# Kernel optimization log

Hardware: AMD Instinct MI355X
Metric: run time of the kernel (lower is better)

The kernel has to match this reference:

```python
import jax, jax.numpy as jnp
import numpy as np
from jax import lax

N = 16384          # total nodes
NUM_GRAPHS = 256   # graphs in the batch
K = 50             # self.knn
NUM_BINS = 5       # num_edge_features
RDF_CUTOFF = 10.0  # Angstrom-scale cutoff for Gaussian RDF smearing
BIG = 1e10         # masked-distance sentinel (finite, jit-safe)


def setup_inputs() -> dict:
    key = jax.random.key(0)
    k1, k2 = jax.random.split(key)
    # 3D pharmacophore coordinates, ~Angstrom scale
    pos = jax.random.normal(k1, (N, 3), dtype=jnp.float32) * 3.0
    # sorted graph-id vector (PyG `batch`)
    batch = jnp.sort(jax.random.randint(k2, (N,), 0, NUM_GRAPHS, dtype=jnp.int64))
    return {"pos": pos, "batch": batch}


def reference(pos, batch):
    n = pos.shape[0]
    # --- brute-force KNN graph (T.KNNGraph, per-graph via batch mask) ---
    sq = jnp.sum(pos * pos, axis=-1)                         # [n]
    d2 = sq[:, None] + sq[None, :] - 2.0 * (pos @ pos.T)     # [n, n]
    same_graph = batch[:, None] == batch[None, :]
    valid = same_graph & ~jnp.eye(n, dtype=bool)             # no self-loops
    d2m = jnp.where(valid, d2, BIG)
    neg_d2, nbr_idx = lax.top_k(-d2m, K)                     # [n, K] nearest by distance
    # symmetric-superset edge list: j -> i (source_to_target flow)
    src = nbr_idx.reshape(-1)                                # [n*K]
    dst = jnp.repeat(jnp.arange(n), K)                       # [n*K]
    edge_index = jnp.stack([src, dst])                       # [2, n*K]
    # --- T.Distance(norm=False): raw Euclidean edge lengths ---
    dist = jnp.sqrt(jnp.maximum(-neg_d2, 1e-12)).reshape(-1)  # [n*K]
    # --- DistanceRDF(num_bins): Gaussian smearing of distances over bins ---
    centers = jnp.linspace(0.0, RDF_CUTOFF, NUM_BINS, dtype=pos.dtype)
    spacing = RDF_CUTOFF / (NUM_BINS - 1)
    gamma = 1.0 / (2.0 * spacing * spacing)
    rdf = jnp.exp(-gamma * (dist[:, None] - centers[None, :]) ** 2)  # [n*K, NUM_BINS]
    return edge_index, dist, rdf
```

## Files before the change

### kernel.cpp

```cpp
#include <hip/hip_runtime.h>
#include <math.h>

#define NTOT  16384
#define NGR   256
#define KNN   50
#define NBINS 5
#define BIGF  1e10f
#define MAXJ  2

__global__ __launch_bounds__(256)
void bounds_kernel(const int* __restrict__ batch, int* __restrict__ bounds)
{
    const int i = blockIdx.x * 256 + threadIdx.x;
    if (i > NTOT) return;
    const int cur  = (i < NTOT) ? batch[i] : NGR;
    const int prev = (i == 0) ? -1 : batch[i - 1];
    for (int t = prev + 1; t <= cur; ++t) bounds[t] = i;
}

__global__ __launch_bounds__(256)
void knn_main(const float* __restrict__ pos,
              const int*   __restrict__ batch,
              const int*   __restrict__ bounds,
              float*       __restrict__ out)
{
    __shared__ unsigned long long keysh[4][2 * 64];

    const int i    = __builtin_amdgcn_readfirstlane((int)(blockIdx.x * 4 + (threadIdx.x >> 6)));
    const int wv   = threadIdx.x >> 6;
    const int lane = threadIdx.x & 63;

    const int g     = batch[i];
    const int start = bounds[g];
    const int end   = bounds[g + 1];
    const int cnt   = end - start;
    const int J     = (cnt + 63) >> 6;

    const float xi = pos[(size_t)i * 3 + 0];
    const float yi = pos[(size_t)i * 3 + 1];
    const float zi = pos[(size_t)i * 3 + 2];
    const float sqi = xi * xi + yi * yi + zi * zi;

    unsigned long long key[MAXJ];
    #pragma unroll
    for (int j = 0; j < MAXJ; ++j) {
        const int c = j * 64 + lane;
        float d2 = BIGF;
        if (j < J && c < cnt && (start + c) != i) {
            const int idx = start + c;
            const float xj = pos[(size_t)idx * 3 + 0];
            const float yj = pos[(size_t)idx * 3 + 1];
            const float zj = pos[(size_t)idx * 3 + 2];
            const float sqj = xj * xj + yj * yj + zj * zj;
            const float dot = xi * xj + yi * yj + zi * zj;
            d2 = sqi + sqj - 2.0f * dot;
        }
        const unsigned int b = __float_as_uint(d2);
        const unsigned int s = ((int)b < 0) ? ~b : (b | 0x80000000u);
        key[j] = ((unsigned long long)s << 32) | (unsigned int)(start + c);
        keysh[wv][c] = key[j];
    }
    __syncthreads();

    int ra[MAXJ] = {0, 0}, rb[MAXJ] = {0, 0};
    {
        const int kpad = (cnt + 7) & ~7;
        const ulonglong2* __restrict__ k2 =
            reinterpret_cast<const ulonglong2*>(&keysh[wv][0]);
        for (int c0 = 0; c0 < kpad; c0 += 8) {
            #pragma unroll
            for (int u = 0; u < 4; ++u) {
                const ulonglong2 kk = k2[(c0 >> 1) + u];
                #pragma unroll
                for (int j = 0; j < MAXJ; ++j) {
                    ra[j] += (kk.x < key[j]);
                    rb[j] += (kk.y < key[j]);
                }
            }
        }
    }
    int rank[MAXJ];
    #pragma unroll
    for (int j = 0; j < MAXJ; ++j) rank[j] = ra[j] + rb[j];

    float* __restrict__ srcO  = out;
    float* __restrict__ dstO  = out + (size_t)NTOT * KNN;
    float* __restrict__ distO = out + (size_t)2 * NTOT * KNN;
    float* __restrict__ rdfO  = out + (size_t)3 * NTOT * KNN;

    const float centers[NBINS] = {0.0f, 2.5f, 5.0f, 7.5f, 10.0f};
    const float gamma = 0.08f;
    const float fi = (float)i;

    #pragma unroll
    for (int j = 0; j < MAXJ; ++j) {
        const int c = j * 64 + lane;
        if (j < J && c < cnt && (start + c) != i && rank[j] < KNN) {
            const unsigned int s  = (unsigned int)(key[j] >> 32);
            const unsigned int b  = (s & 0x80000000u) ? (s & 0x7fffffffu) : ~s;
            const float d2 = __uint_as_float(b);
            const size_t e = (size_t)i * KNN + rank[j];
            srcO[e]  = (float)(start + c);
            dstO[e]  = fi;
            const float d = sqrtf(fmaxf(d2, 1e-12f));
            distO[e] = d;
            #pragma unroll
            for (int bb = 0; bb < NBINS; ++bb) {
                const float dd = d - centers[bb];
                rdfO[e * NBINS + bb] = __expf(-gamma * dd * dd);
            }
        }
    }

    if (cnt <= KNN) {
        const int r = (cnt - 1) + lane;
        if (r < KNN) {
            const int m = lane;
            int jj;
            if (m < start)       jj = m;
            else if (m == start) jj = i;
            else                 jj = end + (m - start - 1);
            const size_t e = (size_t)i * KNN + r;
            srcO[e]  = (float)jj;
            dstO[e]  = fi;
            distO[e] = 100000.0f;
            #pragma unroll
            for (int bb = 0; bb < NBINS; ++bb)
                rdfO[e * NBINS + bb] = 0.0f;
        }
    }
}

extern "C" void kernel_launch(void* const* d_in, const int* in_sizes, int n_in,
                              void* d_out, int out_size, void* d_ws, size_t ws_size,
                              hipStream_t stream) {
    const float* pos    = (const float*)d_in[0];
    const int*   batch  = (const int*)d_in[1];
    float*       out    = (float*)d_out;
    int*         bounds = (int*)d_ws;

    bounds_kernel<<<dim3(65), dim3(256), 0, stream>>>(batch, bounds);
    knn_main<<<dim3(NTOT / 4), dim3(256), 0, stream>>>(pos, batch, bounds, out);
}
```

Baseline: 76.01 us.

## Rank with 32-bit distance keys and fall back to tie-break only on ties

```diff
diff --git a/kernel.cpp b/kernel.cpp
--- a/kernel.cpp
+++ b/kernel.cpp
@@ -18,13 +18,13 @@
     for (int t = prev + 1; t <= cur; ++t) bounds[t] = i;
 }
 
-__global__ __launch_bounds__(256)
+__global__ __launch_bounds__(256, 8)
 void knn_main(const float* __restrict__ pos,
               const int*   __restrict__ batch,
               const int*   __restrict__ bounds,
               float*       __restrict__ out)
 {
-    __shared__ unsigned long long keysh[4][2 * 64];
+    __shared__ unsigned int hish[4][128];
 
     const int i    = __builtin_amdgcn_readfirstlane((int)(blockIdx.x * 4 + (threadIdx.x >> 6)));
     const int wv   = threadIdx.x >> 6;
@@ -41,12 +41,14 @@
     const float zi = pos[(size_t)i * 3 + 2];
     const float sqi = xi * xi + yi * yi + zi * zi;
 
-    unsigned long long key[MAXJ];
+    unsigned int hi[MAXJ];
+    bool valid[MAXJ];
     #pragma unroll
     for (int j = 0; j < MAXJ; ++j) {
         const int c = j * 64 + lane;
+        valid[j] = (j < J) && (c < cnt) && ((start + c) != i);
         float d2 = BIGF;
-        if (j < J && c < cnt && (start + c) != i) {
+        if (valid[j]) {
             const int idx = start + c;
             const float xj = pos[(size_t)idx * 3 + 0];
             const float yj = pos[(size_t)idx * 3 + 1];
@@ -56,32 +58,56 @@
             d2 = sqi + sqj - 2.0f * dot;
         }
         const unsigned int b = __float_as_uint(d2);
-        const unsigned int s = ((int)b < 0) ? ~b : (b | 0x80000000u);
-        key[j] = ((unsigned long long)s << 32) | (unsigned int)(start + c);
-        keysh[wv][c] = key[j];
+        hi[j] = ((int)b < 0) ? ~b : (b | 0x80000000u);
+        hish[wv][c] = hi[j];
     }
     __syncthreads();
 
-    int ra[MAXJ] = {0, 0}, rb[MAXJ] = {0, 0};
+    int rank[MAXJ] = {0, 0};
+    const int kpad = (cnt + 7) & ~7;
+    const uint4* __restrict__ k4 = reinterpret_cast<const uint4*>(&hish[wv][0]);
+    if (J == 1) {
+        int ra = 0, rb = 0;
+        for (int c0 = 0; c0 < kpad; c0 += 8) {
+            const uint4 A = k4[(c0 >> 2) + 0];
+            const uint4 B = k4[(c0 >> 2) + 1];
+            ra += (A.x < hi[0]) + (A.y < hi[0]) + (A.z < hi[0]) + (A.w < hi[0]);
+            rb += (B.x < hi[0]) + (B.y < hi[0]) + (B.z < hi[0]) + (B.w < hi[0]);
+        }
+        rank[0] = ra + rb;
+    } else {
+        int ra0 = 0, rb0 = 0, ra1 = 0, rb1 = 0;
+        for (int c0 = 0; c0 < kpad; c0 += 8) {
+            const uint4 A = k4[(c0 >> 2) + 0];
+            const uint4 B = k4[(c0 >> 2) + 1];
+            ra0 += (A.x < hi[0]) + (A.y < hi[0]) + (A.z < hi[0]) + (A.w < hi[0]);
+            rb0 += (B.x < hi[0]) + (B.y < hi[0]) + (B.z < hi[0]) + (B.w < hi[0]);
+            ra1 += (A.x < hi[1]) + (A.y < hi[1]) + (A.z < hi[1]) + (A.w < hi[1]);
+            rb1 += (B.x < hi[1]) + (B.y < hi[1]) + (B.z < hi[1]) + (B.w < hi[1]);
+        }
+        rank[0] = ra0 + rb0;
+        rank[1] = ra1 + rb1;
+    }
+
     {
-        const int kpad = (cnt + 7) & ~7;
-        const ulonglong2* __restrict__ k2 =
-            reinterpret_cast<const ulonglong2*>(&keysh[wv][0]);
-        for (int c0 = 0; c0 < kpad; c0 += 8) {
+        int s = (valid[0] ? rank[0] : 0) + (valid[1] ? rank[1] : 0);
+        #pragma unroll
+        for (int off = 32; off > 0; off >>= 1) s += __shfl_xor(s, off, 64);
+        const int expect = ((cnt - 1) * (cnt - 2)) >> 1;
+        if (s != expect) {
             #pragma unroll
-            for (int u = 0; u < 4; ++u) {
-                const ulonglong2 kk = k2[(c0 >> 1) + u];
-                #pragma unroll
-                for (int j = 0; j < MAXJ; ++j) {
-                    ra[j] += (kk.x < key[j]);
-                    rb[j] += (kk.y < key[j]);
+            for (int j = 0; j < MAXJ; ++j) {
+                if (!valid[j]) continue;
+                const int c = j * 64 + lane;
+                int r = 0;
+                for (int k = 0; k < cnt; ++k) {
+                    const unsigned int h = hish[wv][k];
+                    r += (h < hi[j]) || (h == hi[j] && k < c);
                 }
+                rank[j] = r;
             }
         }
     }
-    int rank[MAXJ];
-    #pragma unroll
-    for (int j = 0; j < MAXJ; ++j) rank[j] = ra[j] + rb[j];
 
     float* __restrict__ srcO  = out;
     float* __restrict__ dstO  = out + (size_t)NTOT * KNN;
@@ -95,8 +121,8 @@
     #pragma unroll
     for (int j = 0; j < MAXJ; ++j) {
         const int c = j * 64 + lane;
-        if (j < J && c < cnt && (start + c) != i && rank[j] < KNN) {
-            const unsigned int s  = (unsigned int)(key[j] >> 32);
+        if (valid[j] && rank[j] < KNN) {
+            const unsigned int s  = hi[j];
             const unsigned int b  = (s & 0x80000000u) ? (s & 0x7fffffffu) : ~s;
             const float d2 = __uint_as_float(b);
             const size_t e = (size_t)i * KNN + rank[j];
```

Measured after the change: 76.43 us. About the same (+0.5%).
